# Performance work log

Measured on AMD Instinct MI355X. Metric: run time of the kernel, lower is better.

Reference implementation:

```python
import jax, jax.numpy as jnp
import numpy as np

NUM_USER = 1_000_000
K = 10
DIM = 32


def setup_inputs() -> dict:
    key = jax.random.key(0)
    k1, k2, k3 = jax.random.split(key, 3)
    features = jax.random.normal(k1, (NUM_USER, DIM), dtype=jnp.float32)
    user_graph = jax.random.randint(k2, (NUM_USER, K), 0, NUM_USER, dtype=jnp.int64)
    user_matrix = jax.random.uniform(k3, (NUM_USER, K), dtype=jnp.float32)
    return {"features": features, "user_graph": user_graph, "user_matrix": user_matrix}


def reference(features, user_graph, user_matrix):
    # features: [U, D]; user_graph: [U, K] int indices; user_matrix: [U, K] weights
    # u_pre[u, d] = sum_k user_matrix[u, k] * features[user_graph[u, k], d]
    u_features = features[user_graph]                     # [U, K, D] gather
    u_pre = jnp.einsum("uk,ukd->ud", user_matrix, u_features)  # weighted sum over K
    return u_pre
```

## Files before the change

### kernel.cpp

```cpp
#include <hip/hip_runtime.h>
#include <hip/hip_bf16.h>


#define U_COUNT 1000000
#define K_NBR   10
#define D_DIM   32

typedef float f32x4 __attribute__((ext_vector_type(4)));

__global__ __launch_bounds__(256) void user_graph_gather_kernel(
    const float* __restrict__ features,
    const int*   __restrict__ user_graph,
    const float* __restrict__ user_matrix,
    float* __restrict__ out)
{
    int t = blockIdx.x * blockDim.x + threadIdx.x;
    int u = t >> 3;
    int r = t & 7;
    if (u >= U_COUNT) return;

    const int*   gu = user_graph + (long long)u * K_NBR;
    const float* wu = user_matrix + (long long)u * K_NBR;

    int   idx[K_NBR];
    float wk[K_NBR];
#pragma unroll
    for (int k = 0; k < K_NBR; ++k) {
        idx[k] = __builtin_nontemporal_load(gu + k);
        wk[k]  = __builtin_nontemporal_load(wu + k);
    }

    f32x4 acc = (f32x4)(0.f);
#pragma unroll
    for (int k = 0; k < K_NBR; ++k) {
        const f32x4* row = reinterpret_cast<const f32x4*>(
            features + (long long)idx[k] * D_DIM);
        f32x4 v = row[r];
        acc += wk[k] * v;
    }

    f32x4* op = reinterpret_cast<f32x4*>(out) + ((long long)u * 8 + r);
    __builtin_nontemporal_store(acc, op);
}

extern "C" void kernel_launch(void* const* d_in, const int* in_sizes, int n_in,
                              void* d_out, int out_size, void* d_ws, size_t ws_size,
                              hipStream_t stream) {
    const float* features    = (const float*)d_in[0];
    const int*   user_graph  = (const int*)d_in[1];
    const float* user_matrix = (const float*)d_in[2];
    float*       out         = (float*)d_out;

    const int total_threads = U_COUNT * 8;
    const int block = 256;
    const int grid  = (total_threads + block - 1) / block;

    user_graph_gather_kernel<<<grid, block, 0, stream>>>(
        features, user_graph, user_matrix, out);
}
```

Measured before the change: 213.9 us.

## Convert features to fp16 in workspace before gathering to halve gather bytes

Adds a pre-pass that converts the fp32 feature table to fp16 in the workspace, then gathers fp16 rows and accumulates in fp32. This halves the bytes per gathered row and shrinks the table so it is more likely to stay in cache. In exchange it adds a full conversion pass over the table on every call and loses some precision. It falls back to the fp32 kernel when the workspace is too small.

```diff
diff --git a/kernel.cpp b/kernel.cpp
--- a/kernel.cpp
+++ b/kernel.cpp
@@ -1,14 +1,67 @@
 #include <hip/hip_runtime.h>
 #include <hip/hip_bf16.h>
+#include <hip/hip_fp16.h>
 
 
 #define U_COUNT 1000000
 #define K_NBR   10
 #define D_DIM   32
 
-typedef float f32x4 __attribute__((ext_vector_type(4)));
+typedef float    f32x4 __attribute__((ext_vector_type(4)));
+typedef _Float16 f16x4 __attribute__((ext_vector_type(4)));
+typedef _Float16 f16x8 __attribute__((ext_vector_type(8)));
 
-__global__ __launch_bounds__(256) void user_graph_gather_kernel(
+__global__ __launch_bounds__(256) void convert_features_kernel(
+    const float* __restrict__ features, _Float16* __restrict__ feat16)
+{
+    long long i = (long long)blockIdx.x * blockDim.x + threadIdx.x;
+    const f32x4* src = reinterpret_cast<const f32x4*>(features) + i * 2;
+    f32x4 a = __builtin_nontemporal_load(src);
+    f32x4 b = __builtin_nontemporal_load(src + 1);
+    f16x8 h;
+    h[0] = (_Float16)a[0]; h[1] = (_Float16)a[1];
+    h[2] = (_Float16)a[2]; h[3] = (_Float16)a[3];
+    h[4] = (_Float16)b[0]; h[5] = (_Float16)b[1];
+    h[6] = (_Float16)b[2]; h[7] = (_Float16)b[3];
+    reinterpret_cast<f16x8*>(feat16)[i] = h;
+}
+
+__global__ __launch_bounds__(256) void gather_f16_kernel(
+    const _Float16* __restrict__ feat16,
+    const int*   __restrict__ user_graph,
+    const float* __restrict__ user_matrix,
+    float* __restrict__ out)
+{
+    int t = blockIdx.x * blockDim.x + threadIdx.x;
+    int u = t >> 3;
+    int r = t & 7;
+    if (u >= U_COUNT) return;
+
+    const int*   gu = user_graph + u * K_NBR;
+    const float* wu = user_matrix + u * K_NBR;
+
+    int   idx[K_NBR];
+    float wk[K_NBR];
+#pragma unroll
+    for (int k = 0; k < K_NBR; ++k) {
+        idx[k] = __builtin_nontemporal_load(gu + k);
+        wk[k]  = __builtin_nontemporal_load(wu + k);
+    }
+
+    f32x4 acc = (f32x4)(0.f);
+#pragma unroll
+    for (int k = 0; k < K_NBR; ++k) {
+        const f16x4* row = reinterpret_cast<const f16x4*>(
+            feat16 + (long long)idx[k] * D_DIM);
+        f16x4 v = row[r];
+        acc += wk[k] * __builtin_convertvector(v, f32x4);
+    }
+
+    f32x4* op = reinterpret_cast<f32x4*>(out) + ((long long)u * 8 + r);
+    __builtin_nontemporal_store(acc, op);
+}
+
+__global__ __launch_bounds__(256) void gather_f32_kernel(
     const float* __restrict__ features,
     const int*   __restrict__ user_graph,
     const float* __restrict__ user_matrix,
@@ -19,8 +72,8 @@
     int r = t & 7;
     if (u >= U_COUNT) return;
 
-    const int*   gu = user_graph + (long long)u * K_NBR;
-    const float* wu = user_matrix + (long long)u * K_NBR;
+    const int*   gu = user_graph + u * K_NBR;
+    const float* wu = user_matrix + u * K_NBR;
 
     int   idx[K_NBR];
     float wk[K_NBR];
@@ -35,8 +88,7 @@
     for (int k = 0; k < K_NBR; ++k) {
         const f32x4* row = reinterpret_cast<const f32x4*>(
             features + (long long)idx[k] * D_DIM);
-        f32x4 v = row[r];
-        acc += wk[k] * v;
+        acc += wk[k] * row[r];
     }
 
     f32x4* op = reinterpret_cast<f32x4*>(out) + ((long long)u * 8 + r);
@@ -51,10 +103,19 @@
     const float* user_matrix = (const float*)d_in[2];
     float*       out         = (float*)d_out;
 
-    const int total_threads = U_COUNT * 8;
+    const size_t feat16_bytes = (size_t)U_COUNT * D_DIM * sizeof(_Float16);
     const int block = 256;
-    const int grid  = (total_threads + block - 1) / block;
+    const int gather_grid = (U_COUNT * 8 + block - 1) / block;
 
-    user_graph_gather_kernel<<<grid, block, 0, stream>>>(
-        features, user_graph, user_matrix, out);
+    if (ws_size >= feat16_bytes) {
+        _Float16* feat16 = (_Float16*)d_ws;
+        const long long total_f16_threads = (long long)U_COUNT * D_DIM / 8;
+        const int conv_grid = (int)((total_f16_threads + block - 1) / block);
+        convert_features_kernel<<<conv_grid, block, 0, stream>>>(features, feat16);
+        gather_f16_kernel<<<gather_grid, block, 0, stream>>>(
+            feat16, user_graph, user_matrix, out);
+    } else {
+        gather_f32_kernel<<<gather_grid, block, 0, stream>>>(
+            features, user_graph, user_matrix, out);
+    }
 }
```

New measurement: 244.5 us. 14.3% more time.
